# Optimization experiments

Hardware: AMD Instinct MI355X
Metric: run time of the kernel (lower is better)

Reference implementation:

```python
import jax, jax.numpy as jnp
import numpy as np

H, W = 2048, 2048
N = H * W
MEAN_MODULO = 1.0


def setup_inputs() -> dict:
    key = jax.random.key(0)
    k1, k2, k3 = jax.random.split(key, 3)
    pred_E = jax.random.uniform(k1, (N,), dtype=jnp.float32)
    pred_v = jax.random.uniform(k2, (N,), dtype=jnp.float32)
    strain = jax.random.normal(k3, (N, 3), dtype=jnp.float32)
    return {"pred_E": pred_E, "pred_v": pred_v, "strain": strain}


def _conv_valid(x_hw, k_33):
    # x_hw: [H, W] -> NHWC [1,H,W,1]; k_33: [3,3] -> HWIO [3,3,1,1]; cross-correlation, VALID
    x = x_hw[None, :, :, None]
    k = k_33[:, :, None, None]
    y = jax.lax.conv_general_dilated(
        x, k, window_strides=(1, 1), padding="VALID",
        dimension_numbers=("NHWC", "HWIO", "NHWC"))
    return y[0, :, :, 0]  # [H-2, W-2]


def reference(pred_E, pred_v, strain):
    # ---- calculate_stress (closed-form batched plane-stress constitutive law) ----
    v = pred_v
    e0, e1, e2 = strain[:, 0], strain[:, 1], strain[:, 2]
    # strain[i] @ [[1,v,0],[v,1,0],[0,0,(1-v)/2]]
    s0 = e0 + v * e1
    s1 = v * e0 + e1
    s2 = e2 * (1.0 - v) * 0.5
    frac = pred_E / (1.0 - v * v)          # E / (1 - v^2), broadcast over 3 components
    stress = jnp.stack([s0, s1, s2], axis=1) * frac[:, None]  # [N, 3]

    # ---- calculate_loss_r (FD equilibrium residuals via 3x3 stencils) ----
    sum_k = jnp.ones((3, 3), dtype=jnp.float32)
    wx_xx = jnp.array([[-1., -1., -1.], [0., 0., 0.], [1., 1., 1.]], dtype=jnp.float32)
    wx_xy = jnp.array([[1., 0., -1.], [1., 0., -1.], [1., 0., -1.]], dtype=jnp.float32)
    wy_yy = wx_xy
    wy_xy = wx_xx

    E_mat = pred_E.reshape(H, W)
    sxx = stress[:, 0].reshape(H, W)
    syy = stress[:, 1].reshape(H, W)
    sxy = stress[:, 2].reshape(H, W)

    E_conv = _conv_valid(E_mat, sum_k)
    fx = _conv_valid(sxx, wx_xx) + _conv_valid(sxy, wx_xy)
    fy = _conv_valid(syy, wy_yy) + _conv_valid(sxy, wy_xy)

    loss_x = jnp.mean(jnp.abs(fx / E_conv))
    loss_y = jnp.mean(jnp.abs(fy / E_conv))
    loss_e = jnp.abs(jnp.mean(pred_E) - MEAN_MODULO)
    return loss_x + loss_y + loss_e / 100.0
```

## Files before the change

### kernel.cpp

```cpp
#include <hip/hip_runtime.h>
#include <math.h>

#define HH 2048
#define WW 2048
#define TILE 32
#define ROWS 34
#define QC   9
#define LSTRIDE 36
#define NBLK (32 * 64)

__device__ __forceinline__ float rcpf(float x) { return __builtin_amdgcn_rcpf(x); }

struct StageRegs {
    float4 E, V, A, B, C;
    int r, q;
    bool ld;
};

__device__ __forceinline__ void stage_load(
    const float* __restrict__ pred_E, const float* __restrict__ pred_v,
    const float* __restrict__ strain, int r0, int c0, int tid, StageRegs R[2])
{
    #pragma unroll
    for (int it = 0; it < 2; ++it) {
        const int idx = tid + it * 256;
        const int r = idx / QC;
        const int q = idx - r * QC;
        R[it].r = r; R[it].q = q;
        const int gi = r0 + r;
        const int gc = c0 + q * 4;
        const bool a = (idx < ROWS * QC) && (gi < HH) && (gc < WW);
        R[it].ld = a;
        if (a) {
            const int g = gi * WW + gc;
            R[it].E = *(const float4*)(pred_E + g);
            R[it].V = *(const float4*)(pred_v + g);
            const float* sp = strain + 3 * g;
            R[it].A = *(const float4*)(sp);
            R[it].B = *(const float4*)(sp + 4);
            R[it].C = *(const float4*)(sp + 8);
        }
    }
}

__device__ __forceinline__ void stage_math_store(
    StageRegs R[2], float& sumE,
    float (*sE)[LSTRIDE], float (*sxx)[LSTRIDE],
    float (*syy)[LSTRIDE], float (*sxy)[LSTRIDE])
{
    #pragma unroll
    for (int it = 0; it < 2; ++it) {
        if (R[it].ld) {
            const int r = R[it].r, q = R[it].q;
            const float e[4]  = {R[it].E.x, R[it].E.y, R[it].E.z, R[it].E.w};
            const float vv[4] = {R[it].V.x, R[it].V.y, R[it].V.z, R[it].V.w};
            const float s0[4] = {R[it].A.x, R[it].A.w, R[it].B.z, R[it].C.y};
            const float s1[4] = {R[it].A.y, R[it].B.x, R[it].B.w, R[it].C.z};
            const float s2[4] = {R[it].A.z, R[it].B.y, R[it].C.x, R[it].C.w};
            float xx[4], yy[4], xy[4];
            #pragma unroll
            for (int p = 0; p < 4; ++p) {
                const float v  = vv[p];
                const float fr = e[p] * rcpf(1.f - v * v);
                xx[p] = (s0[p] + v * s1[p]) * fr;
                yy[p] = (v * s0[p] + s1[p]) * fr;
                xy[p] = (s2[p] * (1.f - v) * 0.5f) * fr;
            }
            const int cq = 4 * q;
            *(float4*)&sE [r][cq] = R[it].E;
            *(float4*)&sxx[r][cq] = make_float4(xx[0], xx[1], xx[2], xx[3]);
            *(float4*)&syy[r][cq] = make_float4(yy[0], yy[1], yy[2], yy[3]);
            *(float4*)&sxy[r][cq] = make_float4(xy[0], xy[1], xy[2], xy[3]);
            if (r < TILE && q < 8)
                sumE += e[0] + e[1] + e[2] + e[3];
        }
    }
}

__device__ __forceinline__ void stencil(
    int r0, int c0, int tid, float& ax, float& ay,
    float (*sE)[LSTRIDE], float (*sxx)[LSTRIDE],
    float (*syy)[LSTRIDE], float (*sxy)[LSTRIDE])
{
    const int tx = tid & 31;
    const int ty = tid >> 5;
    const int lb = ty * 4;

    float rsE[6], rsxx[6], rsxy[6], xyL[6], xyR[6], yyL[6], yyR[6];
    #pragma unroll
    for (int i = 0; i < 6; ++i) {
        const int r = lb + i;
        rsE[i]  = sE [r][tx] + sE [r][tx + 1] + sE [r][tx + 2];
        rsxx[i] = sxx[r][tx] + sxx[r][tx + 1] + sxx[r][tx + 2];
        const float l = sxy[r][tx], m = sxy[r][tx + 1], rg = sxy[r][tx + 2];
        xyL[i] = l; xyR[i] = rg; rsxy[i] = l + m + rg;
        yyL[i] = syy[r][tx]; yyR[i] = syy[r][tx + 2];
    }

    const bool cok = (c0 + tx) < (WW - 2);
    #pragma unroll
    for (int k = 0; k < 4; ++k) {
        const int gi = r0 + lb + k;
        if (cok && gi < (HH - 2)) {
            const float rEc = rcpf(rsE[k] + rsE[k + 1] + rsE[k + 2]);
            const float fx = (rsxx[k + 2] - rsxx[k])
                           + (xyL[k] + xyL[k + 1] + xyL[k + 2])
                           - (xyR[k] + xyR[k + 1] + xyR[k + 2]);
            const float fy = (yyL[k] + yyL[k + 1] + yyL[k + 2])
                           - (yyR[k] + yyR[k + 1] + yyR[k + 2])
                           + (rsxy[k + 2] - rsxy[k]);
            ax += fabsf(fx) * rEc;
            ay += fabsf(fy) * rEc;
        }
    }
}

__global__ __launch_bounds__(256, 4) void fused_loss_kernel(
    const float* __restrict__ pred_E,
    const float* __restrict__ pred_v,
    const float* __restrict__ strain,
    float* __restrict__ part)
{
    __shared__ float sE [ROWS][LSTRIDE];
    __shared__ float sxx[ROWS][LSTRIDE];
    __shared__ float syy[ROWS][LSTRIDE];
    __shared__ float sxy[ROWS][LSTRIDE];

    const int tid = threadIdx.x;
    const int r0 = blockIdx.y * TILE;
    const int c0 = blockIdx.x * (2 * TILE);

    float sumE = 0.f, ax = 0.f, ay = 0.f;
    StageRegs R0[2], R1[2];

    stage_load(pred_E, pred_v, strain, r0, c0, tid, R0);
    stage_math_store(R0, sumE, sE, sxx, syy, sxy);
    __syncthreads();
    stage_load(pred_E, pred_v, strain, r0, c0 + TILE, tid, R1);
    stencil(r0, c0, tid, ax, ay, sE, sxx, syy, sxy);
    __syncthreads();
    stage_math_store(R1, sumE, sE, sxx, syy, sxy);
    __syncthreads();
    stencil(r0, c0 + TILE, tid, ax, ay, sE, sxx, syy, sxy);

    #pragma unroll
    for (int off = 32; off > 0; off >>= 1) {
        ax   += __shfl_down(ax, off);
        ay   += __shfl_down(ay, off);
        sumE += __shfl_down(sumE, off);
    }
    __shared__ float red[3][4];
    const int wave = tid >> 6, lane = tid & 63;
    if (lane == 0) { red[0][wave] = ax; red[1][wave] = ay; red[2][wave] = sumE; }
    __syncthreads();
    if (tid == 0) {
        const int b = blockIdx.y * 32 + blockIdx.x;
        part[b]            = red[0][0] + red[0][1] + red[0][2] + red[0][3];
        part[NBLK + b]     = red[1][0] + red[1][1] + red[1][2] + red[1][3];
        part[2 * NBLK + b] = red[2][0] + red[2][1] + red[2][2] + red[2][3];
    }
}

__global__ __launch_bounds__(256) void finalize_kernel(
    const float* __restrict__ part, float* __restrict__ out)
{
    const int tid = threadIdx.x;
    const float4* px = (const float4*)(part);
    const float4* py = (const float4*)(part + NBLK);
    const float4* pe = (const float4*)(part + 2 * NBLK);
    float x = 0.f, y = 0.f, e = 0.f;
    #pragma unroll
    for (int k = 0; k < 2; ++k) {
        const int i = tid + k * 256;
        const float4 a = px[i], b = py[i], c = pe[i];
        x += a.x + a.y + a.z + a.w;
        y += b.x + b.y + b.z + b.w;
        e += c.x + c.y + c.z + c.w;
    }
    #pragma unroll
    for (int off = 32; off > 0; off >>= 1) {
        x += __shfl_down(x, off);
        y += __shfl_down(y, off);
        e += __shfl_down(e, off);
    }
    __shared__ float red[3][4];
    const int wave = tid >> 6, lane = tid & 63;
    if (lane == 0) { red[0][wave] = x; red[1][wave] = y; red[2][wave] = e; }
    __syncthreads();
    if (tid == 0) {
        const float rx = red[0][0] + red[0][1] + red[0][2] + red[0][3];
        const float ry = red[1][0] + red[1][1] + red[1][2] + red[1][3];
        const float re = red[2][0] + red[2][1] + red[2][2] + red[2][3];
        const float M = (float)((HH - 2) * (WW - 2));
        const float loss_x = rx / M;
        const float loss_y = ry / M;
        const float loss_e = fabsf(re / (float)(HH * WW) - 1.0f);
        out[0] = loss_x + loss_y + loss_e * 0.01f;
    }
}

extern "C" void kernel_launch(void* const* d_in, const int* in_sizes, int n_in,
                              void* d_out, int out_size, void* d_ws, size_t ws_size,
                              hipStream_t stream) {
    const float* pred_E = (const float*)d_in[0];
    const float* pred_v = (const float*)d_in[1];
    const float* strain = (const float*)d_in[2];
    float* out  = (float*)d_out;
    float* part = (float*)d_ws;

    dim3 grid(WW / (2 * TILE), HH / TILE);
    fused_loss_kernel<<<grid, 256, 0, stream>>>(pred_E, pred_v, strain, part);
    finalize_kernel<<<1, 256, 0, stream>>>(part, out);
}
```

Measured before the change: 110.6 us.

## Process full 34x66 halo tile in one stage with rolling-row stencil

Replaces the two-half staged pipeline (two 32x32 subtiles with a register prefetch of the second half) with a single 34x68 shared tile loaded at once. This removes the duplicated halo columns and the extra barriers. The stencil now gives each thread 8 output rows in a 64-wide layout, using a rolling three-row register window instead of precomputing six rows. In exchange the kernel gives up the overlap of the second tile's global loads with the first stencil, and it uses more shared memory and holds three staged load sets in registers, which may reduce occupancy.

```diff
diff --git a/kernel.cpp b/kernel.cpp
--- a/kernel.cpp
+++ b/kernel.cpp
@@ -3,11 +3,13 @@
 
 #define HH 2048
 #define WW 2048
-#define TILE 32
+#define TILE_H 32
+#define TILE_W 64
 #define ROWS 34
-#define QC   9
-#define LSTRIDE 36
+#define QC   17
+#define LSTRIDE 72
 #define NBLK (32 * 64)
+#define NITEMS (ROWS * QC)
 
 __device__ __forceinline__ float rcpf(float x) { return __builtin_amdgcn_rcpf(x); }
 
@@ -19,17 +21,17 @@
 
 __device__ __forceinline__ void stage_load(
     const float* __restrict__ pred_E, const float* __restrict__ pred_v,
-    const float* __restrict__ strain, int r0, int c0, int tid, StageRegs R[2])
-{
-    #pragma unroll
-    for (int it = 0; it < 2; ++it) {
+    const float* __restrict__ strain, int r0, int c0, int tid, StageRegs R[3])
+{
+    #pragma unroll
+    for (int it = 0; it < 3; ++it) {
         const int idx = tid + it * 256;
         const int r = idx / QC;
         const int q = idx - r * QC;
         R[it].r = r; R[it].q = q;
         const int gi = r0 + r;
         const int gc = c0 + q * 4;
-        const bool a = (idx < ROWS * QC) && (gi < HH) && (gc < WW);
+        const bool a = (idx < NITEMS) && (gi < HH) && (gc < WW);
         R[it].ld = a;
         if (a) {
             const int g = gi * WW + gc;
@@ -44,12 +46,12 @@
 }
 
 __device__ __forceinline__ void stage_math_store(
-    StageRegs R[2], float& sumE,
+    StageRegs R[3], float& sumE,
     float (*sE)[LSTRIDE], float (*sxx)[LSTRIDE],
     float (*syy)[LSTRIDE], float (*sxy)[LSTRIDE])
 {
     #pragma unroll
-    for (int it = 0; it < 2; ++it) {
+    for (int it = 0; it < 3; ++it) {
         if (R[it].ld) {
             const int r = R[it].r, q = R[it].q;
             const float e[4]  = {R[it].E.x, R[it].E.y, R[it].E.z, R[it].E.w};
@@ -71,47 +73,58 @@
             *(float4*)&sxx[r][cq] = make_float4(xx[0], xx[1], xx[2], xx[3]);
             *(float4*)&syy[r][cq] = make_float4(yy[0], yy[1], yy[2], yy[3]);
             *(float4*)&sxy[r][cq] = make_float4(xy[0], xy[1], xy[2], xy[3]);
-            if (r < TILE && q < 8)
+            if (r < TILE_H && q < 16)
                 sumE += e[0] + e[1] + e[2] + e[3];
         }
     }
 }
 
+__device__ __forceinline__ void row7(
+    int r, int tx, float* o,
+    const float (*sE)[LSTRIDE], const float (*sxx)[LSTRIDE],
+    const float (*syy)[LSTRIDE], const float (*sxy)[LSTRIDE])
+{
+    o[0] = sE [r][tx] + sE [r][tx + 1] + sE [r][tx + 2];
+    o[1] = sxx[r][tx] + sxx[r][tx + 1] + sxx[r][tx + 2];
+    const float l = sxy[r][tx], m = sxy[r][tx + 1], rg = sxy[r][tx + 2];
+    o[2] = l + m + rg;
+    o[3] = l;
+    o[4] = rg;
+    o[5] = syy[r][tx];
+    o[6] = syy[r][tx + 2];
+}
+
 __device__ __forceinline__ void stencil(
     int r0, int c0, int tid, float& ax, float& ay,
-    float (*sE)[LSTRIDE], float (*sxx)[LSTRIDE],
-    float (*syy)[LSTRIDE], float (*sxy)[LSTRIDE])
-{
-    const int tx = tid & 31;
-    const int ty = tid >> 5;
-    const int lb = ty * 4;
-
-    float rsE[6], rsxx[6], rsxy[6], xyL[6], xyR[6], yyL[6], yyR[6];
-    #pragma unroll
-    for (int i = 0; i < 6; ++i) {
-        const int r = lb + i;
-        rsE[i]  = sE [r][tx] + sE [r][tx + 1] + sE [r][tx + 2];
-        rsxx[i] = sxx[r][tx] + sxx[r][tx + 1] + sxx[r][tx + 2];
-        const float l = sxy[r][tx], m = sxy[r][tx + 1], rg = sxy[r][tx + 2];
-        xyL[i] = l; xyR[i] = rg; rsxy[i] = l + m + rg;
-        yyL[i] = syy[r][tx]; yyR[i] = syy[r][tx + 2];
-    }
+    const float (*sE)[LSTRIDE], const float (*sxx)[LSTRIDE],
+    const float (*syy)[LSTRIDE], const float (*sxy)[LSTRIDE])
+{
+    const int tx = tid & 63;
+    const int ty = tid >> 6;
+    const int lb = ty * 8;
+
+    float w0[7], w1[7], w2[7];
+    row7(lb + 0, tx, w0, sE, sxx, syy, sxy);
+    row7(lb + 1, tx, w1, sE, sxx, syy, sxy);
 
     const bool cok = (c0 + tx) < (WW - 2);
     #pragma unroll
-    for (int k = 0; k < 4; ++k) {
+    for (int k = 0; k < 8; ++k) {
+        row7(lb + k + 2, tx, w2, sE, sxx, syy, sxy);
         const int gi = r0 + lb + k;
         if (cok && gi < (HH - 2)) {
-            const float rEc = rcpf(rsE[k] + rsE[k + 1] + rsE[k + 2]);
-            const float fx = (rsxx[k + 2] - rsxx[k])
-                           + (xyL[k] + xyL[k + 1] + xyL[k + 2])
-                           - (xyR[k] + xyR[k + 1] + xyR[k + 2]);
-            const float fy = (yyL[k] + yyL[k + 1] + yyL[k + 2])
-                           - (yyR[k] + yyR[k + 1] + yyR[k + 2])
-                           + (rsxy[k + 2] - rsxy[k]);
+            const float rEc = rcpf(w0[0] + w1[0] + w2[0]);
+            const float fx = (w2[1] - w0[1])
+                           + (w0[3] + w1[3] + w2[3])
+                           - (w0[4] + w1[4] + w2[4]);
+            const float fy = (w0[5] + w1[5] + w2[5])
+                           - (w0[6] + w1[6] + w2[6])
+                           + (w2[2] - w0[2]);
             ax += fabsf(fx) * rEc;
             ay += fabsf(fy) * rEc;
         }
+        #pragma unroll
+        for (int j = 0; j < 7; ++j) { w0[j] = w1[j]; w1[j] = w2[j]; }
     }
 }
 
@@ -127,21 +140,16 @@
     __shared__ float sxy[ROWS][LSTRIDE];
 
     const int tid = threadIdx.x;
-    const int r0 = blockIdx.y * TILE;
-    const int c0 = blockIdx.x * (2 * TILE);
+    const int r0 = blockIdx.y * TILE_H;
+    const int c0 = blockIdx.x * TILE_W;
 
     float sumE = 0.f, ax = 0.f, ay = 0.f;
-    StageRegs R0[2], R1[2];
-
-    stage_load(pred_E, pred_v, strain, r0, c0, tid, R0);
-    stage_math_store(R0, sumE, sE, sxx, syy, sxy);
-    __syncthreads();
-    stage_load(pred_E, pred_v, strain, r0, c0 + TILE, tid, R1);
+    StageRegs R[3];
+
+    stage_load(pred_E, pred_v, strain, r0, c0, tid, R);
+    stage_math_store(R, sumE, sE, sxx, syy, sxy);
+    __syncthreads();
     stencil(r0, c0, tid, ax, ay, sE, sxx, syy, sxy);
-    __syncthreads();
-    stage_math_store(R1, sumE, sE, sxx, syy, sxy);
-    __syncthreads();
-    stencil(r0, c0 + TILE, tid, ax, ay, sE, sxx, syy, sxy);
 
     #pragma unroll
     for (int off = 32; off > 0; off >>= 1) {
@@ -151,6 +159,7 @@
     }
     __shared__ float red[3][4];
     const int wave = tid >> 6, lane = tid & 63;
+    __syncthreads();
     if (lane == 0) { red[0][wave] = ax; red[1][wave] = ay; red[2][wave] = sumE; }
     __syncthreads();
     if (tid == 0) {
@@ -208,7 +217,7 @@
     float* out  = (float*)d_out;
     float* part = (float*)d_ws;
 
-    dim3 grid(WW / (2 * TILE), HH / TILE);
+    dim3 grid(WW / TILE_W, HH / TILE_H);
     fused_loss_kernel<<<grid, 256, 0, stream>>>(pred_E, pred_v, strain, part);
     finalize_kernel<<<1, 256, 0, stream>>>(part, out);
 }
```

Measured after the change: 108.9 us. Within noise of the previous version (-1.5%).
